# Kernel tuning notes

Measured on AMD Instinct MI355X. Metric: run time of the kernel, lower is better.

The kernel has to match this reference:

```python
import jax, jax.numpy as jnp
import numpy as np

B, T, N, E = 8, 32, 128, 2048
IN_DIM, HID, OUT = 512, 512, 512
SLOPE = 0.2  # GATConv default negative_slope


def setup_inputs() -> dict:
    key = jax.random.key(0)
    ks = jax.random.split(key, 12)
    x = jax.random.normal(ks[0], (B, T, N, IN_DIM), jnp.float32)
    edge_index = jax.random.randint(ks[1], (B, T, 2, E), 0, N)
    valid_step_index = jax.random.randint(ks[2], (B,), 1, T + 1)
    def lin(k, o, i):
        return jax.random.normal(k, (o, i), jnp.float32) / np.sqrt(i).astype(np.float32)
    W1 = lin(ks[3], HID, IN_DIM)
    a1_src = jax.random.normal(ks[4], (HID,), jnp.float32) / np.sqrt(HID).astype(np.float32)
    a1_dst = jax.random.normal(ks[5], (HID,), jnp.float32) / np.sqrt(HID).astype(np.float32)
    b1 = jnp.zeros((HID,), jnp.float32)
    W2 = lin(ks[6], OUT, HID)
    a2_src = jax.random.normal(ks[7], (OUT,), jnp.float32) / np.sqrt(OUT).astype(np.float32)
    a2_dst = jax.random.normal(ks[8], (OUT,), jnp.float32) / np.sqrt(OUT).astype(np.float32)
    b2 = jnp.zeros((OUT,), jnp.float32)
    W_time = jax.random.normal(ks[9], (T, T), jnp.float32) / np.sqrt(T).astype(np.float32)
    b_time = jnp.zeros((T,), jnp.float32)
    return dict(x=x, edge_index=edge_index, valid_step_index=valid_step_index,
                W1=W1, a1_src=a1_src, a1_dst=a1_dst, b1=b1,
                W2=W2, a2_src=a2_src, a2_dst=a2_dst, b2=b2,
                W_time=W_time, b_time=b_time)


def _gat(x, src, dst, W, a_src, a_dst, b):
    # Single-head PyG GATConv (concat=True, heads=1), self-loops already appended.
    n = x.shape[0]
    h = x @ W.T                                             # [N, H]
    e = jax.nn.leaky_relu((h @ a_src)[src] + (h @ a_dst)[dst], SLOPE)  # [E]
    m = jax.ops.segment_max(e, dst, num_segments=n)
    m = jnp.where(jnp.isfinite(m), m, 0.0)
    p = jnp.exp(e - m[dst])
    denom = jax.ops.segment_sum(p, dst, num_segments=n)
    alpha = p / denom[dst]                                  # segment softmax over incoming edges
    return jax.ops.segment_sum(h[src] * alpha[:, None], dst, num_segments=n) + b


def reference(x, edge_index, valid_step_index, W1, a1_src, a1_dst, b1,
              W2, a2_src, a2_dst, b2, W_time, b_time):
    b_, t_, n_, _ = x.shape
    g = b_ * t_
    xf = x.reshape(g, n_, -1)
    ei = edge_index.reshape(g, 2, -1)
    # add self loops (PyG GATConv default add_self_loops=True)
    loops = jnp.broadcast_to(jnp.arange(n_)[None, None, :], (g, 2, n_))
    ei = jnp.concatenate([ei, loops], axis=-1)
    src, dst = ei[:, 0], ei[:, 1]
    gat = jax.vmap(_gat, in_axes=(0, 0, 0, None, None, None, None))
    h = jax.nn.gelu(gat(xf, src, dst, W1, a1_src, a1_dst, b1), approximate=False)
    # F.dropout(p=0.2) is identity in eval mode
    h = gat(h, src, dst, W2, a2_src, a2_dst, b2)
    y = h.reshape(b_, t_, n_, -1)
    mask = (jnp.arange(t_)[None, :] < valid_step_index[:, None]).astype(y.dtype)
    y = y * mask[:, :, None, None]
    # TemporalConv: Conv2d(T, T, 1) over time-as-channel = linear mix across time, then GELU, residual
    fused = jax.nn.gelu(jnp.einsum('ts,bsnf->btnf', W_time, y)
                        + b_time[None, :, None, None], approximate=False)
    return fused + y
```

## Files before the change

kernel.cpp:

```cpp
#include <hip/hip_runtime.h>

using u16 = unsigned short;
using u32 = unsigned int;

typedef __bf16 bf16x8 __attribute__((ext_vector_type(8)));
typedef float  f32x4  __attribute__((ext_vector_type(4)));

__device__ __forceinline__ u16 f2bf(float f) {
    u32 u = __float_as_uint(f);
    u32 r = u + 0x7fffu + ((u >> 16) & 1u);
    return (u16)(r >> 16);
}
__device__ __forceinline__ float gelu_f(float x) {
    return 0.5f * x * (1.0f + erff(x * 0.70710678118654752440f));
}

#define GLOAD16(gp, lp) __builtin_amdgcn_global_load_lds( \
    (const __attribute__((address_space(1))) void*)(gp),  \
    (__attribute__((address_space(3))) void*)(lp), 16, 0, 0)
#define WAITV(n) asm volatile("s_waitcnt vmcnt(" #n ")" ::: "memory")
#define WAITL0   asm volatile("s_waitcnt lgkmcnt(0)" ::: "memory")

__global__ __launch_bounds__(256) void prep_kernel(
    const float* __restrict__ W1, const float* __restrict__ W2,
    u16* __restrict__ W1b, u16* __restrict__ W2b)
{
    int i = blockIdx.x * 256 + threadIdx.x;
    const float* src = (i < 65536) ? W1 : W2;
    u16* dst = (i < 65536) ? W1b : W2b;
    int ii = i & 65535;
    int f = ii >> 7;
    int k = (ii & 127) * 4;
    float4 v = ((const float4*)src)[ii];
    int kd = (k & ~31) | ((((k >> 3) & 3) ^ (f & 3)) << 3) | (k & 7);
    ushort4 o;
    o.x = f2bf(v.x); o.y = f2bf(v.y); o.z = f2bf(v.z); o.w = f2bf(v.w);
    *(ushort4*)&dst[f * 512 + kd] = o;
}

__global__ __launch_bounds__(512, 2) void mega_kernel(
    const float* __restrict__ x, const int* __restrict__ ei, const int* __restrict__ valid,
    const u16* __restrict__ W1b, const float* __restrict__ a1s, const float* __restrict__ a1d,
    const float* __restrict__ b1,
    const u16* __restrict__ W2b, const float* __restrict__ a2s, const float* __restrict__ a2d,
    const float* __restrict__ b2,
    float* __restrict__ outF)
{
    __shared__ u16 Hs[65536];
    __shared__ __align__(16) u16 SG[16384];
    u32*   cntw = (u32*)SG;
    u16*   ring = SG + 4096;
    float* stf  = (float*)(SG + 12288);

    const int tid  = threadIdx.x;
    const int lane = tid & 63;
    const int w    = tid >> 6;
    const int rl   = lane & 15;
    const int grp  = lane >> 4;
    const int gid  = blockIdx.x;
    const int bb   = gid >> 5, tt = gid & 31;

    const int4* es = (const int4*)(ei + (size_t)gid * 4096);
    int4 e0 = es[tid], e1 = es[512 + tid];

    for (int i = tid; i < 2048; i += 512) cntw[i] = 0u;
    stf[tid] = 0.f;

    const float4* xg = (const float4*)(x + (size_t)gid * 65536);
    #pragma unroll
    for (int it = 0; it < 16; ++it) {
        float4 a = xg[tid * 2 + it * 1024];
        float4 b = xg[tid * 2 + 1 + it * 1024];
        int m = it * 8 + w;
        int sp = lane ^ ((lane >> 3) & 7) ^ (m & 7);
        ushort4 lo, hi;
        lo.x = f2bf(a.x); lo.y = f2bf(a.y); lo.z = f2bf(a.z); lo.w = f2bf(a.w);
        hi.x = f2bf(b.x); hi.y = f2bf(b.y); hi.z = f2bf(b.z); hi.w = f2bf(b.w);
        *(ushort4*)&Hs[m * 512 + sp * 8]     = lo;
        *(ushort4*)&Hs[m * 512 + sp * 8 + 4] = hi;
    }
    __syncthreads();

    atomicAdd(&cntw[e1.x * 16 + (e0.x >> 3)], 1u << ((e0.x & 7) * 4));
    atomicAdd(&cntw[e1.y * 16 + (e0.y >> 3)], 1u << ((e0.y & 7) * 4));
    atomicAdd(&cntw[e1.z * 16 + (e0.z >> 3)], 1u << ((e0.z & 7) * 4));
    atomicAdd(&cntw[e1.w * 16 + (e0.w >> 3)], 1u << ((e0.w & 7) * 4));
    if (tid < 128) atomicAdd(&cntw[tid * 16 + (tid >> 3)], 1u << ((tid & 7) * 4));
    __syncthreads();

    u16* myring = ring + w * 1024;

    for (int L = 0; L < 2; ++L) {
        const u16*  WL  = L ? W2b : W1b;
        const float* av_s = L ? a2s : a1s;
        const float* av_d = L ? a2d : a1d;

        f32x4 acc[8][4] = {};
        {
            auto STAGEW = [&](int q) {
                int kt2 = q >> 2, j2 = q & 3;
                const u16* src = WL + (size_t)(w * 64 + j2 * 16 + (lane >> 2)) * 512
                               + kt2 * 32 + (lane & 3) * 8;
                GLOAD16(src, &myring[(q & 1) * 512]);
            };
            STAGEW(0); STAGEW(1);
            for (int kt = 0; kt < 16; ++kt) {
                bf16x8 af[8];
                #pragma unroll
                for (int i = 0; i < 8; ++i) {
                    int m = i * 16 + rl;
                    int sp = (kt * 4 + grp) ^ (kt >> 1) ^ (m & 7);
                    af[i] = *(const bf16x8*)&Hs[m * 512 + sp * 8];
                }
                #pragma unroll
                for (int j = 0; j < 4; ++j) {
                    int q = kt * 4 + j;
                    if (kt == 15 && j == 3) { WAITV(0); } else { WAITV(1); }
                    bf16x8 bv = *(const bf16x8*)&myring[(q & 1) * 512 + rl * 32 + ((grp ^ (rl & 3)) * 8)];
                    WAITL0;
                    __builtin_amdgcn_sched_barrier(0);
                    if (q + 2 < 64) STAGEW(q + 2);
                    #pragma unroll
                    for (int i = 0; i < 8; ++i)
                        acc[i][j] = __builtin_amdgcn_mfma_f32_16x16x32_bf16(af[i], bv, acc[i][j], 0, 0, 0);
                }
            }
        }
        __syncthreads();

        {
            float asv[4], adv[4];
            #pragma unroll
            for (int j = 0; j < 4; ++j) {
                int f = w * 64 + j * 16 + rl;
                asv[j] = av_s[f]; adv[j] = av_d[f];
            }
            #pragma unroll
            for (int i = 0; i < 8; ++i) {
                #pragma unroll
                for (int j = 0; j < 4; ++j) {
                    int f = j * 16 + rl + w * 64;
                    int oct = i * 2 + (grp >> 1);
                    int elem = f * 128 + ((oct ^ (f & 15)) * 8) + (grp & 1) * 4;
                    ushort4 o;
                    o.x = f2bf(acc[i][j][0]); o.y = f2bf(acc[i][j][1]);
                    o.z = f2bf(acc[i][j][2]); o.w = f2bf(acc[i][j][3]);
                    *(ushort4*)&Hs[elem] = o;
                }
                #pragma unroll
                for (int r = 0; r < 4; ++r) {
                    float s = acc[i][0][r] * asv[0] + acc[i][1][r] * asv[1]
                            + acc[i][2][r] * asv[2] + acc[i][3][r] * asv[3];
                    float d = acc[i][0][r] * adv[0] + acc[i][1][r] * adv[1]
                            + acc[i][2][r] * adv[2] + acc[i][3][r] * adv[3];
                    #pragma unroll
                    for (int off = 1; off < 16; off <<= 1) {
                        s += __shfl_xor(s, off);
                        d += __shfl_xor(d, off);
                    }
                    if (rl == 0) {
                        int m = i * 16 + grp * 4 + r;
                        atomicAdd(&stf[m], s);
                        atomicAdd(&stf[128 + m], d);
                    }
                }
            }
        }
        __syncthreads();

        for (int r = 0; r < 16; ++r) {
            int m = w * 16 + r;
            float sdm = stf[128 + m];
            u32 w0 = cntw[m * 16 + (lane >> 3)];
            u32 w1 = cntw[m * 16 + 8 + (lane >> 3)];
            u32 c0 = (w0 >> ((lane & 7) * 4)) & 15u;
            u32 c1 = (w1 >> ((lane & 7) * 4)) & 15u;
            float E0 = stf[lane] + sdm;      E0 = E0 > 0.f ? E0 : 0.2f * E0;
            float E1 = stf[lane + 64] + sdm; E1 = E1 > 0.f ? E1 : 0.2f * E1;
            float mx = fmaxf(c0 ? E0 : -1e30f, c1 ? E1 : -1e30f);
            #pragma unroll
            for (int off = 1; off < 64; off <<= 1) mx = fmaxf(mx, __shfl_xor(mx, off));
            float p = (c0 ? (float)c0 * __expf(E0 - mx) : 0.f)
                    + (c1 ? (float)c1 * __expf(E1 - mx) : 0.f);
            #pragma unroll
            for (int off = 1; off < 64; off <<= 1) p += __shfl_xor(p, off);
            if (lane == 0) { stf[256 + m] = mx; stf[384 + m] = 1.f / p; }
        }
        __syncthreads();

        f32x4 acc2[32] = {};
        {
            int m = w * 16 + rl;
            float sdm = stf[128 + m], Mm = stf[256 + m], rDm = stf[384 + m];
            bf16x8 pa[4];
            #pragma unroll
            for (int kb = 0; kb < 4; ++kb) {
                u32 word = cntw[m * 16 + kb * 4 + grp];
                #pragma unroll
                for (int e = 0; e < 8; ++e) {
                    u32 c = (word >> (e * 4)) & 15u;
                    int s = kb * 32 + grp * 8 + e;
                    float ev = stf[s] + sdm; ev = ev > 0.f ? ev : 0.2f * ev;
                    float p = c ? (float)c * __expf(ev - Mm) * rDm : 0.f;
                    pa[kb][e] = (__bf16)p;
                }
            }
            #pragma unroll
            for (int j = 0; j < 32; ++j) {
                int f = j * 16 + rl;
                #pragma unroll
                for (int kb = 0; kb < 4; ++kb) {
                    bf16x8 hb = *(const bf16x8*)&Hs[f * 128 + (((kb * 4 + grp) ^ rl) * 8)];
                    acc2[j] = __builtin_amdgcn_mfma_f32_16x16x32_bf16(pa[kb], hb, acc2[j], 0, 0, 0);
                }
            }
        }
        __syncthreads();

        if (L == 0) {
            stf[tid] = 0.f;
            #pragma unroll
            for (int j = 0; j < 32; ++j) {
                int f = j * 16 + rl;
                float bv = b1[f];
                int slot = f >> 3;
                #pragma unroll
                for (int r = 0; r < 4; ++r) {
                    int m2 = w * 16 + grp * 4 + r;
                    int loc = slot ^ ((slot >> 3) & 7) ^ (m2 & 7);
                    Hs[m2 * 512 + loc * 8 + (f & 7)] = f2bf(gelu_f(acc2[j][r] + bv));
                }
            }
            __syncthreads();
        } else {
            float msk = (tt < valid[bb]) ? 1.f : 0.f;
            float* og = outF + (size_t)gid * 65536;
            #pragma unroll
            for (int j = 0; j < 32; ++j) {
                int f = j * 16 + rl;
                float bv = b2[f];
                #pragma unroll
                for (int r = 0; r < 4; ++r) {
                    int m2 = w * 16 + grp * 4 + r;
                    og[m2 * 512 + f] = (acc2[j][r] + bv) * msk;
                }
            }
        }
    }
}

__global__ __launch_bounds__(256) void timemix_kernel(float* __restrict__ y,
                                                      const float* __restrict__ Wt,
                                                      const float* __restrict__ bt) {
    __shared__ float wsm[1024];
    __shared__ float bts[32];
    int tid = threadIdx.x;
    for (int i = tid; i < 1024; i += 256) wsm[i] = Wt[i];
    if (tid < 32) bts[tid] = bt[tid];
    __syncthreads();
    int blk = blockIdx.x;
    int b = blk >> 8;
    int rem = blk & 255;
    int n = rem >> 1;
    int f = (rem & 1) * 256 + tid;
    size_t base = ((size_t)b * 4096 + n) * 512 + f;
    float ys[32];
    #pragma unroll
    for (int s = 0; s < 32; ++s) ys[s] = y[base + (size_t)s * 65536];
    #pragma unroll
    for (int t = 0; t < 32; ++t) {
        float a = bts[t];
        #pragma unroll
        for (int s = 0; s < 32; ++s) a += wsm[t * 32 + s] * ys[s];
        y[base + (size_t)t * 65536] = gelu_f(a) + ys[t];
    }
}

extern "C" void kernel_launch(void* const* d_in, const int* in_sizes, int n_in,
                              void* d_out, int out_size, void* d_ws, size_t ws_size,
                              hipStream_t stream) {
    const float* x     = (const float*)d_in[0];
    const int*   ei    = (const int*)d_in[1];
    const int*   valid = (const int*)d_in[2];
    const float* W1    = (const float*)d_in[3];
    const float* a1s   = (const float*)d_in[4];
    const float* a1d   = (const float*)d_in[5];
    const float* b1    = (const float*)d_in[6];
    const float* W2    = (const float*)d_in[7];
    const float* a2s   = (const float*)d_in[8];
    const float* a2d   = (const float*)d_in[9];
    const float* b2    = (const float*)d_in[10];
    const float* Wt    = (const float*)d_in[11];
    const float* bt    = (const float*)d_in[12];
    float* out = (float*)d_out;

    char* ws = (char*)d_ws;
    u16* W1b = (u16*)(ws);
    u16* W2b = (u16*)(ws + 524288);

    prep_kernel<<<512, 256, 0, stream>>>(W1, W2, W1b, W2b);
    mega_kernel<<<256, 512, 0, stream>>>(x, ei, valid,
        W1b, a1s, a1d, b1, W2b, a2s, a2d, b2, out);
    timemix_kernel<<<2048, 256, 0, stream>>>(out, Wt, bt);
}
```

Before: 218.1 us.

## Load GAT weights directly into registers instead of LDS ring staging

Removes the per-wave LDS ring buffer fed by global_load_lds. The weight B-fragments are now read directly from global memory into a 4-deep register prefetch queue, and the prep kernel stops swizzling the weight layout. It also raises MFMA priority with s_setprio, drops launch bounds to 1 block per CU, and splits the layer-2 aggregation into 4 chunks of 8 accumulators so the epilogue writes out sooner with fewer live registers. The aim is to cut LDS traffic and waitcnt stalls, at the cost of lower occupancy and uncoalesced 16-byte global reads from L2.

```diff
diff --git a/kernel.cpp b/kernel.cpp
--- a/kernel.cpp
+++ b/kernel.cpp
@@ -14,12 +14,6 @@
 __device__ __forceinline__ float gelu_f(float x) {
     return 0.5f * x * (1.0f + erff(x * 0.70710678118654752440f));
 }
-
-#define GLOAD16(gp, lp) __builtin_amdgcn_global_load_lds( \
-    (const __attribute__((address_space(1))) void*)(gp),  \
-    (__attribute__((address_space(3))) void*)(lp), 16, 0, 0)
-#define WAITV(n) asm volatile("s_waitcnt vmcnt(" #n ")" ::: "memory")
-#define WAITL0   asm volatile("s_waitcnt lgkmcnt(0)" ::: "memory")
 
 __global__ __launch_bounds__(256) void prep_kernel(
     const float* __restrict__ W1, const float* __restrict__ W2,
@@ -29,16 +23,13 @@
     const float* src = (i < 65536) ? W1 : W2;
     u16* dst = (i < 65536) ? W1b : W2b;
     int ii = i & 65535;
-    int f = ii >> 7;
-    int k = (ii & 127) * 4;
     float4 v = ((const float4*)src)[ii];
-    int kd = (k & ~31) | ((((k >> 3) & 3) ^ (f & 3)) << 3) | (k & 7);
     ushort4 o;
     o.x = f2bf(v.x); o.y = f2bf(v.y); o.z = f2bf(v.z); o.w = f2bf(v.w);
-    *(ushort4*)&dst[f * 512 + kd] = o;
-}
-
-__global__ __launch_bounds__(512, 2) void mega_kernel(
+    ((ushort4*)dst)[ii] = o;
+}
+
+__global__ __launch_bounds__(512, 1) void mega_kernel(
     const float* __restrict__ x, const int* __restrict__ ei, const int* __restrict__ valid,
     const u16* __restrict__ W1b, const float* __restrict__ a1s, const float* __restrict__ a1d,
     const float* __restrict__ b1,
@@ -47,10 +38,9 @@
     float* __restrict__ outF)
 {
     __shared__ u16 Hs[65536];
-    __shared__ __align__(16) u16 SG[16384];
+    __shared__ __align__(16) u16 SG[8192];
     u32*   cntw = (u32*)SG;
-    u16*   ring = SG + 4096;
-    float* stf  = (float*)(SG + 12288);
+    float* stf  = (float*)(SG + 4096);
 
     const int tid  = threadIdx.x;
     const int lane = tid & 63;
@@ -88,22 +78,18 @@
     if (tid < 128) atomicAdd(&cntw[tid * 16 + (tid >> 3)], 1u << ((tid & 7) * 4));
     __syncthreads();
 
-    u16* myring = ring + w * 1024;
-
     for (int L = 0; L < 2; ++L) {
-        const u16*  WL  = L ? W2b : W1b;
+        const u16*  WL   = L ? W2b : W1b;
         const float* av_s = L ? a2s : a1s;
         const float* av_d = L ? a2d : a1d;
 
         f32x4 acc[8][4] = {};
         {
-            auto STAGEW = [&](int q) {
-                int kt2 = q >> 2, j2 = q & 3;
-                const u16* src = WL + (size_t)(w * 64 + j2 * 16 + (lane >> 2)) * 512
-                               + kt2 * 32 + (lane & 3) * 8;
-                GLOAD16(src, &myring[(q & 1) * 512]);
-            };
-            STAGEW(0); STAGEW(1);
+            const u16* wg = WL + (size_t)(w * 64 + rl) * 512 + grp * 8;
+            bf16x8 wreg[4];
+            #pragma unroll
+            for (int q = 0; q < 4; ++q)
+                wreg[q] = *(const bf16x8*)&wg[(q & 3) * 16 * 512 + (q >> 2) * 32];
             for (int kt = 0; kt < 16; ++kt) {
                 bf16x8 af[8];
                 #pragma unroll
@@ -115,14 +101,16 @@
                 #pragma unroll
                 for (int j = 0; j < 4; ++j) {
                     int q = kt * 4 + j;
-                    if (kt == 15 && j == 3) { WAITV(0); } else { WAITV(1); }
-                    bf16x8 bv = *(const bf16x8*)&myring[(q & 1) * 512 + rl * 32 + ((grp ^ (rl & 3)) * 8)];
-                    WAITL0;
-                    __builtin_amdgcn_sched_barrier(0);
-                    if (q + 2 < 64) STAGEW(q + 2);
+                    bf16x8 bv = wreg[j];
+                    if (q + 4 < 64) {
+                        int qn = q + 4;
+                        wreg[j] = *(const bf16x8*)&wg[(qn & 3) * 16 * 512 + (qn >> 2) * 32];
+                    }
+                    __builtin_amdgcn_s_setprio(1);
                     #pragma unroll
                     for (int i = 0; i < 8; ++i)
                         acc[i][j] = __builtin_amdgcn_mfma_f32_16x16x32_bf16(af[i], bv, acc[i][j], 0, 0, 0);
+                    __builtin_amdgcn_s_setprio(0);
                 }
             }
         }
@@ -188,23 +176,24 @@
         }
         __syncthreads();
 
-        f32x4 acc2[32] = {};
-        {
-            int m = w * 16 + rl;
-            float sdm = stf[128 + m], Mm = stf[256 + m], rDm = stf[384 + m];
-            bf16x8 pa[4];
-            #pragma unroll
-            for (int kb = 0; kb < 4; ++kb) {
-                u32 word = cntw[m * 16 + kb * 4 + grp];
-                #pragma unroll
-                for (int e = 0; e < 8; ++e) {
-                    u32 c = (word >> (e * 4)) & 15u;
-                    int s = kb * 32 + grp * 8 + e;
-                    float ev = stf[s] + sdm; ev = ev > 0.f ? ev : 0.2f * ev;
-                    float p = c ? (float)c * __expf(ev - Mm) * rDm : 0.f;
-                    pa[kb][e] = (__bf16)p;
-                }
-            }
+        int m = w * 16 + rl;
+        float sdm = stf[128 + m], Mm = stf[256 + m], rDm = stf[384 + m];
+        bf16x8 pa[4];
+        #pragma unroll
+        for (int kb = 0; kb < 4; ++kb) {
+            u32 word = cntw[m * 16 + kb * 4 + grp];
+            #pragma unroll
+            for (int e = 0; e < 8; ++e) {
+                u32 c = (word >> (e * 4)) & 15u;
+                int s = kb * 32 + grp * 8 + e;
+                float ev = stf[s] + sdm; ev = ev > 0.f ? ev : 0.2f * ev;
+                float p = c ? (float)c * __expf(ev - Mm) * rDm : 0.f;
+                pa[kb][e] = (__bf16)p;
+            }
+        }
+
+        if (L == 0) {
+            f32x4 acc2[32] = {};
             #pragma unroll
             for (int j = 0; j < 32; ++j) {
                 int f = j * 16 + rl;
@@ -214,10 +203,7 @@
                     acc2[j] = __builtin_amdgcn_mfma_f32_16x16x32_bf16(pa[kb], hb, acc2[j], 0, 0, 0);
                 }
             }
-        }
-        __syncthreads();
-
-        if (L == 0) {
+            __syncthreads();
             stf[tid] = 0.f;
             #pragma unroll
             for (int j = 0; j < 32; ++j) {
@@ -236,13 +222,26 @@
             float msk = (tt < valid[bb]) ? 1.f : 0.f;
             float* og = outF + (size_t)gid * 65536;
             #pragma unroll
-            for (int j = 0; j < 32; ++j) {
-                int f = j * 16 + rl;
-                float bv = b2[f];
-                #pragma unroll
-                for (int r = 0; r < 4; ++r) {
-                    int m2 = w * 16 + grp * 4 + r;
-                    og[m2 * 512 + f] = (acc2[j][r] + bv) * msk;
+            for (int jb = 0; jb < 4; ++jb) {
+                f32x4 acc2[8] = {};
+                #pragma unroll
+                for (int j8 = 0; j8 < 8; ++j8) {
+                    int f = (jb * 8 + j8) * 16 + rl;
+                    #pragma unroll
+                    for (int kb = 0; kb < 4; ++kb) {
+                        bf16x8 hb = *(const bf16x8*)&Hs[f * 128 + (((kb * 4 + grp) ^ rl) * 8)];
+                        acc2[j8] = __builtin_amdgcn_mfma_f32_16x16x32_bf16(pa[kb], hb, acc2[j8], 0, 0, 0);
+                    }
+                }
+                #pragma unroll
+                for (int j8 = 0; j8 < 8; ++j8) {
+                    int f = (jb * 8 + j8) * 16 + rl;
+                    float bv = b2[f];
+                    #pragma unroll
+                    for (int r = 0; r < 4; ++r) {
+                        int m2 = w * 16 + grp * 4 + r;
+                        og[m2 * 512 + f] = (acc2[j8][r] + bv) * msk;
+                    }
                 }
             }
         }
```

Result: slower. 303.3 us (+39.1%).

## Split fused GAT mega-kernel into separate GEMM and aggregation kernels

Applied to the files above, without the earlier changes.

Replaces the single per-graph mega kernel, which kept features in LDS across both GAT layers, with separate kernels: a bf16 conversion pass over x, a projection GEMM run twice (two blocks per graph, each covering half the output features, with fp32 weights converted to bf16 on the fly), and an aggregation kernel per layer. The split aims to raise parallelism and occupancy beyond the 256 large-LDS blocks of the fused design. In exchange, intermediate bf16 activations and transposed H now round-trip through global memory (tens of MB per layer), there are more launches, and attention scores are accumulated with global atomics.

```diff
diff --git a/kernel.cpp b/kernel.cpp
--- a/kernel.cpp
+++ b/kernel.cpp
@@ -18,66 +18,155 @@
 #define GLOAD16(gp, lp) __builtin_amdgcn_global_load_lds( \
     (const __attribute__((address_space(1))) void*)(gp),  \
     (__attribute__((address_space(3))) void*)(lp), 16, 0, 0)
-#define WAITV(n) asm volatile("s_waitcnt vmcnt(" #n ")" ::: "memory")
-#define WAITL0   asm volatile("s_waitcnt lgkmcnt(0)" ::: "memory")
 
 __global__ __launch_bounds__(256) void prep_kernel(
-    const float* __restrict__ W1, const float* __restrict__ W2,
-    u16* __restrict__ W1b, u16* __restrict__ W2b)
+    const float* __restrict__ x, u16* __restrict__ Xb, float* __restrict__ Z)
 {
-    int i = blockIdx.x * 256 + threadIdx.x;
-    const float* src = (i < 65536) ? W1 : W2;
-    u16* dst = (i < 65536) ? W1b : W2b;
-    int ii = i & 65535;
-    int f = ii >> 7;
-    int k = (ii & 127) * 4;
-    float4 v = ((const float4*)src)[ii];
-    int kd = (k & ~31) | ((((k >> 3) & 3) ^ (f & 3)) << 3) | (k & 7);
-    ushort4 o;
-    o.x = f2bf(v.x); o.y = f2bf(v.y); o.z = f2bf(v.z); o.w = f2bf(v.w);
-    *(ushort4*)&dst[f * 512 + kd] = o;
-}
-
-__global__ __launch_bounds__(512, 2) void mega_kernel(
-    const float* __restrict__ x, const int* __restrict__ ei, const int* __restrict__ valid,
-    const u16* __restrict__ W1b, const float* __restrict__ a1s, const float* __restrict__ a1d,
-    const float* __restrict__ b1,
-    const u16* __restrict__ W2b, const float* __restrict__ a2s, const float* __restrict__ a2d,
-    const float* __restrict__ b2,
-    float* __restrict__ outF)
+    const int i0 = blockIdx.x * 256 + threadIdx.x;
+    const int stride = gridDim.x * 256;
+    if (i0 < 32768) ((float4*)Z)[i0] = make_float4(0.f, 0.f, 0.f, 0.f);
+    for (int i = i0; i < 4194304; i += stride) {
+        float4 v = ((const float4*)x)[i];
+        ushort4 o;
+        o.x = f2bf(v.x); o.y = f2bf(v.y); o.z = f2bf(v.z); o.w = f2bf(v.w);
+        ((ushort4*)Xb)[i] = o;
+    }
+}
+
+__global__ __launch_bounds__(512) void gat_gemm(
+    const u16* __restrict__ A, const float* __restrict__ W,
+    const float* __restrict__ a_s, const float* __restrict__ a_d,
+    u16* __restrict__ HT, float* __restrict__ SS, float* __restrict__ SD)
 {
-    __shared__ u16 Hs[65536];
-    __shared__ __align__(16) u16 SG[16384];
-    u32*   cntw = (u32*)SG;
-    u16*   ring = SG + 4096;
-    float* stf  = (float*)(SG + 12288);
+    __shared__ __align__(16) u16 As[2][128 * 32];
+    __shared__ float sA[128], dA[128];
 
     const int tid  = threadIdx.x;
     const int lane = tid & 63;
     const int w    = tid >> 6;
     const int rl   = lane & 15;
     const int grp  = lane >> 4;
-    const int gid  = blockIdx.x;
-    const int bb   = gid >> 5, tt = gid & 31;
-
-    const int4* es = (const int4*)(ei + (size_t)gid * 4096);
+    const int g    = blockIdx.x >> 1;
+    const int hf   = blockIdx.x & 1;
+
+    if (tid < 128) { sA[tid] = 0.f; dA[tid] = 0.f; }
+
+    const u16* Ag   = A + (size_t)g * 65536;
+    const u16* asrc = Ag + (size_t)(w * 16 + (lane >> 2)) * 512 + (lane & 3) * 8;
+    const float* wg = W + (size_t)(hf * 256 + w * 32 + rl) * 512 + grp * 8;
+
+    float4 wf0[2], wf1[2];
+    wf0[0] = *(const float4*)&wg[0];     wf1[0] = *(const float4*)&wg[4];
+    wf0[1] = *(const float4*)&wg[8192];  wf1[1] = *(const float4*)&wg[8192 + 4];
+
+    GLOAD16(asrc, &As[0][w * 512]);
+    __syncthreads();
+
+    f32x4 acc[8][2] = {};
+    int buf = 0;
+    for (int kt = 0; kt < 16; ++kt) {
+        if (kt < 15) GLOAD16(asrc + (kt + 1) * 32, &As[buf ^ 1][w * 512]);
+        bf16x8 wb[2];
+        #pragma unroll
+        for (int j = 0; j < 2; ++j) {
+            float4 lo = wf0[j], hi = wf1[j];
+            wb[j][0] = (__bf16)lo.x; wb[j][1] = (__bf16)lo.y;
+            wb[j][2] = (__bf16)lo.z; wb[j][3] = (__bf16)lo.w;
+            wb[j][4] = (__bf16)hi.x; wb[j][5] = (__bf16)hi.y;
+            wb[j][6] = (__bf16)hi.z; wb[j][7] = (__bf16)hi.w;
+        }
+        if (kt < 15) {
+            #pragma unroll
+            for (int j = 0; j < 2; ++j) {
+                wf0[j] = *(const float4*)&wg[j * 8192 + (kt + 1) * 32];
+                wf1[j] = *(const float4*)&wg[j * 8192 + (kt + 1) * 32 + 4];
+            }
+        }
+        #pragma unroll
+        for (int i = 0; i < 8; ++i) {
+            bf16x8 af = *(const bf16x8*)&As[buf][(i * 16 + rl) * 32 + grp * 8];
+            acc[i][0] = __builtin_amdgcn_mfma_f32_16x16x32_bf16(af, wb[0], acc[i][0], 0, 0, 0);
+            acc[i][1] = __builtin_amdgcn_mfma_f32_16x16x32_bf16(af, wb[1], acc[i][1], 0, 0, 0);
+        }
+        __syncthreads();
+        buf ^= 1;
+    }
+
+    float asv[2], adv[2];
+    #pragma unroll
+    for (int j = 0; j < 2; ++j) {
+        int f = hf * 256 + w * 32 + j * 16 + rl;
+        asv[j] = a_s[f]; adv[j] = a_d[f];
+    }
+    u16* Hg = HT + (size_t)g * 65536;
+    #pragma unroll
+    for (int i = 0; i < 8; ++i) {
+        #pragma unroll
+        for (int j = 0; j < 2; ++j) {
+            int f = hf * 256 + w * 32 + j * 16 + rl;
+            int node0 = i * 16 + grp * 4;
+            ushort4 o;
+            o.x = f2bf(acc[i][j][0]); o.y = f2bf(acc[i][j][1]);
+            o.z = f2bf(acc[i][j][2]); o.w = f2bf(acc[i][j][3]);
+            *(ushort4*)&Hg[(size_t)f * 128 + node0] = o;
+        }
+        #pragma unroll
+        for (int r = 0; r < 4; ++r) {
+            float s = acc[i][0][r] * asv[0] + acc[i][1][r] * asv[1];
+            float d = acc[i][0][r] * adv[0] + acc[i][1][r] * adv[1];
+            #pragma unroll
+            for (int off = 1; off < 16; off <<= 1) {
+                s += __shfl_xor(s, off);
+                d += __shfl_xor(d, off);
+            }
+            if (rl == 0) {
+                int node = i * 16 + grp * 4 + r;
+                atomicAdd(&sA[node], s);
+                atomicAdd(&dA[node], d);
+            }
+        }
+    }
+    __syncthreads();
+    if (tid < 128) {
+        atomicAdd(&SS[g * 128 + tid], sA[tid]);
+        atomicAdd(&SD[g * 128 + tid], dA[tid]);
+    }
+}
+
+template<int MODE>
+__global__ __launch_bounds__(512) void gat_agg(
+    const u16* __restrict__ HT, const int* __restrict__ ei,
+    const float* __restrict__ SS, const float* __restrict__ SD,
+    const float* __restrict__ bias, const int* __restrict__ valid,
+    u16* __restrict__ outU, float* __restrict__ outF)
+{
+    __shared__ u16 Hts[65536];
+    __shared__ u32 cntw[2048];
+    __shared__ float stf[512];
+
+    const int tid  = threadIdx.x;
+    const int lane = tid & 63;
+    const int w    = tid >> 6;
+    const int rl   = lane & 15;
+    const int grp  = lane >> 4;
+    const int g    = blockIdx.x;
+    const int bb   = g >> 5, tt = g & 31;
+
+    const int4* es = (const int4*)(ei + (size_t)g * 4096);
     int4 e0 = es[tid], e1 = es[512 + tid];
 
+    const u16* Hg = HT + (size_t)g * 65536;
+    #pragma unroll
+    for (int it = 0; it < 16; ++it) {
+        int f = it * 32 + (tid >> 4);
+        int blk = tid & 15;
+        GLOAD16(Hg + (size_t)f * 128 + ((blk ^ (f & 15)) * 8), &Hts[it * 4096 + w * 512]);
+    }
+
     for (int i = tid; i < 2048; i += 512) cntw[i] = 0u;
-    stf[tid] = 0.f;
-
-    const float4* xg = (const float4*)(x + (size_t)gid * 65536);
-    #pragma unroll
-    for (int it = 0; it < 16; ++it) {
-        float4 a = xg[tid * 2 + it * 1024];
-        float4 b = xg[tid * 2 + 1 + it * 1024];
-        int m = it * 8 + w;
-        int sp = lane ^ ((lane >> 3) & 7) ^ (m & 7);
-        ushort4 lo, hi;
-        lo.x = f2bf(a.x); lo.y = f2bf(a.y); lo.z = f2bf(a.z); lo.w = f2bf(a.w);
-        hi.x = f2bf(b.x); hi.y = f2bf(b.y); hi.z = f2bf(b.z); hi.w = f2bf(b.w);
-        *(ushort4*)&Hs[m * 512 + sp * 8]     = lo;
-        *(ushort4*)&Hs[m * 512 + sp * 8 + 4] = hi;
+    if (tid < 128) {
+        stf[tid]       = SS[g * 128 + tid];
+        stf[128 + tid] = SD[g * 128 + tid];
     }
     __syncthreads();
 
@@ -88,162 +177,66 @@
     if (tid < 128) atomicAdd(&cntw[tid * 16 + (tid >> 3)], 1u << ((tid & 7) * 4));
     __syncthreads();
 
-    u16* myring = ring + w * 1024;
-
-    for (int L = 0; L < 2; ++L) {
-        const u16*  WL  = L ? W2b : W1b;
-        const float* av_s = L ? a2s : a1s;
-        const float* av_d = L ? a2d : a1d;
-
-        f32x4 acc[8][4] = {};
-        {
-            auto STAGEW = [&](int q) {
-                int kt2 = q >> 2, j2 = q & 3;
-                const u16* src = WL + (size_t)(w * 64 + j2 * 16 + (lane >> 2)) * 512
-                               + kt2 * 32 + (lane & 3) * 8;
-                GLOAD16(src, &myring[(q & 1) * 512]);
-            };
-            STAGEW(0); STAGEW(1);
-            for (int kt = 0; kt < 16; ++kt) {
-                bf16x8 af[8];
-                #pragma unroll
-                for (int i = 0; i < 8; ++i) {
-                    int m = i * 16 + rl;
-                    int sp = (kt * 4 + grp) ^ (kt >> 1) ^ (m & 7);
-                    af[i] = *(const bf16x8*)&Hs[m * 512 + sp * 8];
-                }
-                #pragma unroll
-                for (int j = 0; j < 4; ++j) {
-                    int q = kt * 4 + j;
-                    if (kt == 15 && j == 3) { WAITV(0); } else { WAITV(1); }
-                    bf16x8 bv = *(const bf16x8*)&myring[(q & 1) * 512 + rl * 32 + ((grp ^ (rl & 3)) * 8)];
-                    WAITL0;
-                    __builtin_amdgcn_sched_barrier(0);
-                    if (q + 2 < 64) STAGEW(q + 2);
-                    #pragma unroll
-                    for (int i = 0; i < 8; ++i)
-                        acc[i][j] = __builtin_amdgcn_mfma_f32_16x16x32_bf16(af[i], bv, acc[i][j], 0, 0, 0);
-                }
-            }
-        }
-        __syncthreads();
-
-        {
-            float asv[4], adv[4];
-            #pragma unroll
-            for (int j = 0; j < 4; ++j) {
-                int f = w * 64 + j * 16 + rl;
-                asv[j] = av_s[f]; adv[j] = av_d[f];
-            }
-            #pragma unroll
-            for (int i = 0; i < 8; ++i) {
-                #pragma unroll
-                for (int j = 0; j < 4; ++j) {
-                    int f = j * 16 + rl + w * 64;
-                    int oct = i * 2 + (grp >> 1);
-                    int elem = f * 128 + ((oct ^ (f & 15)) * 8) + (grp & 1) * 4;
-                    ushort4 o;
-                    o.x = f2bf(acc[i][j][0]); o.y = f2bf(acc[i][j][1]);
-                    o.z = f2bf(acc[i][j][2]); o.w = f2bf(acc[i][j][3]);
-                    *(ushort4*)&Hs[elem] = o;
-                }
-                #pragma unroll
-                for (int r = 0; r < 4; ++r) {
-                    float s = acc[i][0][r] * asv[0] + acc[i][1][r] * asv[1]
-                            + acc[i][2][r] * asv[2] + acc[i][3][r] * asv[3];
-                    float d = acc[i][0][r] * adv[0] + acc[i][1][r] * adv[1]
-                            + acc[i][2][r] * adv[2] + acc[i][3][r] * adv[3];
-                    #pragma unroll
-                    for (int off = 1; off < 16; off <<= 1) {
-                        s += __shfl_xor(s, off);
-                        d += __shfl_xor(d, off);
-                    }
-                    if (rl == 0) {
-                        int m = i * 16 + grp * 4 + r;
-                        atomicAdd(&stf[m], s);
-                        atomicAdd(&stf[128 + m], d);
-                    }
-                }
-            }
-        }
-        __syncthreads();
-
-        for (int r = 0; r < 16; ++r) {
-            int m = w * 16 + r;
-            float sdm = stf[128 + m];
-            u32 w0 = cntw[m * 16 + (lane >> 3)];
-            u32 w1 = cntw[m * 16 + 8 + (lane >> 3)];
-            u32 c0 = (w0 >> ((lane & 7) * 4)) & 15u;
-            u32 c1 = (w1 >> ((lane & 7) * 4)) & 15u;
-            float E0 = stf[lane] + sdm;      E0 = E0 > 0.f ? E0 : 0.2f * E0;
-            float E1 = stf[lane + 64] + sdm; E1 = E1 > 0.f ? E1 : 0.2f * E1;
-            float mx = fmaxf(c0 ? E0 : -1e30f, c1 ? E1 : -1e30f);
-            #pragma unroll
-            for (int off = 1; off < 64; off <<= 1) mx = fmaxf(mx, __shfl_xor(mx, off));
-            float p = (c0 ? (float)c0 * __expf(E0 - mx) : 0.f)
-                    + (c1 ? (float)c1 * __expf(E1 - mx) : 0.f);
-            #pragma unroll
-            for (int off = 1; off < 64; off <<= 1) p += __shfl_xor(p, off);
-            if (lane == 0) { stf[256 + m] = mx; stf[384 + m] = 1.f / p; }
-        }
-        __syncthreads();
-
-        f32x4 acc2[32] = {};
-        {
-            int m = w * 16 + rl;
-            float sdm = stf[128 + m], Mm = stf[256 + m], rDm = stf[384 + m];
-            bf16x8 pa[4];
+    for (int r = 0; r < 16; ++r) {
+        int m = w * 16 + r;
+        float sdm = stf[128 + m];
+        u32 w0 = cntw[m * 16 + (lane >> 3)];
+        u32 w1 = cntw[m * 16 + 8 + (lane >> 3)];
+        u32 c0 = (w0 >> ((lane & 7) * 4)) & 15u;
+        u32 c1 = (w1 >> ((lane & 7) * 4)) & 15u;
+        float E0 = stf[lane] + sdm;      E0 = E0 > 0.f ? E0 : 0.2f * E0;
+        float E1 = stf[lane + 64] + sdm; E1 = E1 > 0.f ? E1 : 0.2f * E1;
+        float mx = fmaxf(c0 ? E0 : -1e30f, c1 ? E1 : -1e30f);
+        #pragma unroll
+        for (int off = 1; off < 64; off <<= 1) mx = fmaxf(mx, __shfl_xor(mx, off));
+        float p = (c0 ? (float)c0 * __expf(E0 - mx) : 0.f)
+                + (c1 ? (float)c1 * __expf(E1 - mx) : 0.f);
+        #pragma unroll
+        for (int off = 1; off < 64; off <<= 1) p += __shfl_xor(p, off);
+        if (lane == 0) { stf[256 + m] = mx; stf[384 + m] = 1.f / p; }
+    }
+    __syncthreads();
+
+    const int m = w * 16 + rl;
+    const float sdm = stf[128 + m], Mm = stf[256 + m], rDm = stf[384 + m];
+    bf16x8 pa[4];
+    #pragma unroll
+    for (int kb = 0; kb < 4; ++kb) {
+        u32 word = cntw[m * 16 + kb * 4 + grp];
+        #pragma unroll
+        for (int e = 0; e < 8; ++e) {
+            u32 c = (word >> (e * 4)) & 15u;
+            int s = kb * 32 + grp * 8 + e;
+            float ev = stf[s] + sdm; ev = ev > 0.f ? ev : 0.2f * ev;
+            float p = c ? (float)c * __expf(ev - Mm) * rDm : 0.f;
+            pa[kb][e] = (__bf16)p;
+        }
+    }
+
+    const float msk = (MODE == 1) ? ((tt < valid[bb]) ? 1.f : 0.f) : 1.f;
+    #pragma unroll 1
+    for (int jc = 0; jc < 8; ++jc) {
+        f32x4 acc2[4] = {};
+        #pragma unroll
+        for (int j4 = 0; j4 < 4; ++j4) {
+            int f = jc * 64 + j4 * 16 + rl;
             #pragma unroll
             for (int kb = 0; kb < 4; ++kb) {
-                u32 word = cntw[m * 16 + kb * 4 + grp];
-                #pragma unroll
-                for (int e = 0; e < 8; ++e) {
-                    u32 c = (word >> (e * 4)) & 15u;
-                    int s = kb * 32 + grp * 8 + e;
-                    float ev = stf[s] + sdm; ev = ev > 0.f ? ev : 0.2f * ev;
-                    float p = c ? (float)c * __expf(ev - Mm) * rDm : 0.f;
-                    pa[kb][e] = (__bf16)p;
-                }
-            }
+                bf16x8 hb = *(const bf16x8*)&Hts[f * 128 + (((kb * 4 + grp) ^ (f & 15)) * 8)];
+                acc2[j4] = __builtin_amdgcn_mfma_f32_16x16x32_bf16(pa[kb], hb, acc2[j4], 0, 0, 0);
+            }
+        }
+        #pragma unroll
+        for (int j4 = 0; j4 < 4; ++j4) {
+            int f = jc * 64 + j4 * 16 + rl;
+            float bv = bias[f];
             #pragma unroll
-            for (int j = 0; j < 32; ++j) {
-                int f = j * 16 + rl;
-                #pragma unroll
-                for (int kb = 0; kb < 4; ++kb) {
-                    bf16x8 hb = *(const bf16x8*)&Hs[f * 128 + (((kb * 4 + grp) ^ rl) * 8)];
-                    acc2[j] = __builtin_amdgcn_mfma_f32_16x16x32_bf16(pa[kb], hb, acc2[j], 0, 0, 0);
-                }
-            }
-        }
-        __syncthreads();
-
-        if (L == 0) {
-            stf[tid] = 0.f;
-            #pragma unroll
-            for (int j = 0; j < 32; ++j) {
-                int f = j * 16 + rl;
-                float bv = b1[f];
-                int slot = f >> 3;
-                #pragma unroll
-                for (int r = 0; r < 4; ++r) {
-                    int m2 = w * 16 + grp * 4 + r;
-                    int loc = slot ^ ((slot >> 3) & 7) ^ (m2 & 7);
-                    Hs[m2 * 512 + loc * 8 + (f & 7)] = f2bf(gelu_f(acc2[j][r] + bv));
-                }
-            }
-            __syncthreads();
-        } else {
-            float msk = (tt < valid[bb]) ? 1.f : 0.f;
-            float* og = outF + (size_t)gid * 65536;
-            #pragma unroll
-            for (int j = 0; j < 32; ++j) {
-                int f = j * 16 + rl;
-                float bv = b2[f];
-                #pragma unroll
-                for (int r = 0; r < 4; ++r) {
-                    int m2 = w * 16 + grp * 4 + r;
-                    og[m2 * 512 + f] = (acc2[j][r] + bv) * msk;
-                }
+            for (int r = 0; r < 4; ++r) {
+                int m2 = w * 16 + grp * 4 + r;
+                if (MODE == 0)
+                    outU[(size_t)g * 65536 + m2 * 512 + f] = f2bf(gelu_f(acc2[j4][r] + bv));
+                else
+                    outF[(size_t)g * 65536 + m2 * 512 + f] = (acc2[j4][r] + bv) * msk;
             }
         }
     }
@@ -295,11 +288,20 @@
     float* out = (float*)d_out;
 
     char* ws = (char*)d_ws;
-    u16* W1b = (u16*)(ws);
-    u16* W2b = (u16*)(ws + 524288);
-
-    prep_kernel<<<512, 256, 0, stream>>>(W1, W2, W1b, W2b);
-    mega_kernel<<<256, 512, 0, stream>>>(x, ei, valid,
-        W1b, a1s, a1d, b1, W2b, a2s, a2d, b2, out);
+    u16* Xb    = (u16*)(ws);
+    u16* HTb   = (u16*)(ws + 33554432);
+    float* SS1 = (float*)(ws + 67108864);
+    float* SD1 = (float*)(ws + 67239936);
+    float* SS2 = (float*)(ws + 67371008);
+    float* SD2 = (float*)(ws + 67502080);
+
+    prep_kernel<<<2048, 256, 0, stream>>>(x, Xb, SS1);
+
+    gat_gemm<<<512, 512, 0, stream>>>(Xb, W1, a1s, a1d, HTb, SS1, SD1);
+    gat_agg<0><<<256, 512, 0, stream>>>(HTb, ei, SS1, SD1, b1, nullptr, Xb, nullptr);
+
+    gat_gemm<<<512, 512, 0, stream>>>(Xb, W2, a2s, a2d, HTb, SS2, SD2);
+    gat_agg<1><<<256, 512, 0, stream>>>(HTb, ei, SS2, SD2, b2, valid, nullptr, out);
+
     timemix_kernel<<<2048, 256, 0, stream>>>(out, Wt, bt);
 }
```

New measurement: 220.2 us. About the same (+1.0%).
